# Optimization experiments

Hardware: AMD Instinct MI355X
Metric: run time of the kernel (lower is better)

Reference implementation:

```python
import jax, jax.numpy as jnp
import numpy as np

N = 100000      # num vertices
NE = 20000      # num hyperedges
NNZ = 1600000   # incidence pairs
NFEAT = 128
NHID = 64       # nhid * nhead = 8 * 8
NCLASS = 40
NLAYER = 4
ALPHA = 0.1
LAMDA = 0.5


def setup_inputs() -> dict:
    key = jax.random.key(0)
    ks = jax.random.split(key, 9)
    x = jax.random.normal(ks[0], (N, NFEAT), dtype=jnp.float32)
    vertex = jax.random.randint(ks[1], (NNZ,), 0, N, dtype=jnp.int32)
    edges = jax.random.randint(ks[2], (NNZ,), 0, NE, dtype=jnp.int32)
    degE = jax.random.uniform(ks[3], (NE, 1), dtype=jnp.float32)
    degV = jax.random.uniform(ks[4], (N, 1), dtype=jnp.float32)
    W0 = jax.random.normal(ks[5], (NFEAT, NHID), dtype=jnp.float32) * 0.05
    b0 = jnp.zeros((NHID,), jnp.float32)
    Ws = jax.random.normal(ks[6], (NLAYER, NHID, NHID), dtype=jnp.float32) * 0.05
    Wout = jax.random.normal(ks[7], (NHID, NCLASS), dtype=jnp.float32) * 0.05
    bout = jnp.zeros((NCLASS,), jnp.float32)
    return dict(x=x, degE=degE, degV=degV, W0=W0, b0=b0, Ws=Ws,
                Wout=Wout, bout=bout, vertex=vertex, edges=edges)


def _normalize_l2(X):
    # torch: norm computed on detached X, inf scales zeroed
    norm = jnp.linalg.norm(jax.lax.stop_gradient(X), axis=1, keepdims=True)
    scale = jnp.where(norm > 0, 1.0 / norm, 0.0)
    return X * scale


def reference(x, degE, degV, W0, b0, Ws, Wout, bout, vertex, edges):
    # per-hyperedge member counts for the 'mean' first_aggregate
    counts = jax.ops.segment_sum(jnp.ones((NNZ,), x.dtype), edges, num_segments=NE)
    counts = jnp.maximum(counts, 1.0)[:, None]  # [NE,1]

    X = jax.nn.relu(x @ W0 + b0)   # [N, NHID]
    X0 = X
    for i in range(NLAYER):
        beta = float(np.log(LAMDA / (i + 1) + 1.0))
        Xve = X[vertex]                                                   # [NNZ, NHID]
        Xe = jax.ops.segment_sum(Xve, edges, num_segments=NE) / counts   # vertex->edge mean
        Xe = Xe * degE                                                    # [NE, NHID]
        Xev = Xe[edges]                                                   # [NNZ, NHID]
        Xv = jax.ops.segment_sum(Xev, vertex, num_segments=N) * degV     # edge->vertex sum
        Xn = _normalize_l2(Xv)                                            # use_norm=True
        Xi = (1.0 - ALPHA) * Xn + ALPHA * X0
        X = jax.nn.relu((1.0 - beta) * Xi + beta * (Xi @ Ws[i]))
    logits = X @ Wout + bout
    return jax.nn.log_softmax(logits, axis=1)
```

## Files before the change

kernel.cpp:

```cpp
#include <hip/hip_runtime.h>
#include <math.h>

constexpr int NV   = 100000;
constexpr int NEg  = 20000;
constexpr int NNZp = 1600000;
constexpr int NF   = 128;
constexpr int NH   = 64;
constexpr int NC   = 40;

constexpr int WE  = 64;
constexpr int NBE = (NEg + WE - 1) / WE;
constexpr int WV  = 256;
constexpr int NBV = (NV + WV - 1) / WV;
constexpr int CAPS = 6400;
constexpr int CH   = 2048;
constexpr int PBLK = (NNZp + CH - 1) / CH;

typedef __bf16 bf16x8 __attribute__((ext_vector_type(8)));
typedef float  f32x4  __attribute__((ext_vector_type(4)));

__device__ __forceinline__ float bf2f(unsigned short u) {
    unsigned int x = ((unsigned int)u) << 16;
    return __builtin_bit_cast(float, x);
}
__device__ __forceinline__ unsigned short f2bf(float f) {
    unsigned int x = __builtin_bit_cast(unsigned int, f);
    x += 0x7fffu + ((x >> 16) & 1u);
    return (unsigned short)(x >> 16);
}
__device__ __forceinline__ ushort4 pack4(float a, float b, float c, float d) {
    ushort4 u; u.x = f2bf(a); u.y = f2bf(b); u.z = f2bf(c); u.w = f2bf(d);
    return u;
}

__global__ __launch_bounds__(256) void coarse_hist(const int* __restrict__ vertex,
                                                   const int* __restrict__ edges,
                                                   int* __restrict__ cnt_be,
                                                   int* __restrict__ cnt_bv) {
    __shared__ int he[NBE], hv[NBV];
    for (int i = threadIdx.x; i < NBE; i += 256) he[i] = 0;
    for (int i = threadIdx.x; i < NBV; i += 256) hv[i] = 0;
    __syncthreads();
    const int base = blockIdx.x * CH;
    const int end  = min(base + CH, NNZp);
    for (int i = base + threadIdx.x; i < end; i += 256) {
        atomicAdd(&he[edges[i]  >> 6], 1);
        atomicAdd(&hv[vertex[i] >> 8], 1);
    }
    __syncthreads();
    for (int i = threadIdx.x; i < NBE; i += 256) if (he[i]) atomicAdd(&cnt_be[i], he[i]);
    for (int i = threadIdx.x; i < NBV; i += 256) if (hv[i]) atomicAdd(&cnt_bv[i], hv[i]);
}

__global__ __launch_bounds__(512) void scan_buckets(const int* __restrict__ cnt_be,
                                                    const int* __restrict__ cnt_bv,
                                                    int* __restrict__ rsb_e,
                                                    int* __restrict__ rsb_v,
                                                    int* __restrict__ rs_e,
                                                    int* __restrict__ rs_v) {
    __shared__ int s[512];
    const int n      = (blockIdx.x == 0) ? NBE : NBV;
    const int* c     = (blockIdx.x == 0) ? cnt_be : cnt_bv;
    int* r           = (blockIdx.x == 0) ? rsb_e : rsb_v;
    const int t = threadIdx.x;
    int v = (t < n) ? c[t] : 0;
    s[t] = v;
    __syncthreads();
    for (int o = 1; o < 512; o <<= 1) {
        int u = (t >= o) ? s[t - o] : 0;
        __syncthreads();
        s[t] += u;
        __syncthreads();
    }
    if (t < n) r[t] = s[t] - v;
    if (t == 0) {
        r[n] = NNZp;
        if (blockIdx.x == 0) rs_e[NEg] = NNZp;
        else                 rs_v[NV]  = NNZp;
    }
}

__global__ __launch_bounds__(256) void partition_both(const int* __restrict__ vertex,
                                                      const int* __restrict__ edges,
                                                      const int* __restrict__ rsb_e,
                                                      const int* __restrict__ rsb_v,
                                                      int* __restrict__ gcur_e,
                                                      int* __restrict__ gcur_v,
                                                      int* __restrict__ vid_out,
                                                      int* __restrict__ eid_out) {
    __shared__ int se[CH], sv[CH];
    __shared__ int cur_e[NBE], cur_v[NBV];
    const int tid = threadIdx.x;
    for (int i = tid; i < NBE; i += 256) cur_e[i] = 0;
    for (int i = tid; i < NBV; i += 256) cur_v[i] = 0;
    __syncthreads();
    const int base = blockIdx.x * CH;
    const int n    = min(base + CH, NNZp) - base;
    for (int i = tid; i < n; i += 256) {
        int e = edges[base + i];
        int v = vertex[base + i];
        se[i] = e; sv[i] = v;
        atomicAdd(&cur_e[e >> 6], 1);
        atomicAdd(&cur_v[v >> 8], 1);
    }
    __syncthreads();
    for (int i = tid; i < NBE; i += 256) {
        int h = cur_e[i];
        cur_e[i] = rsb_e[i] + (h ? atomicAdd(&gcur_e[i], h) : 0);
    }
    for (int i = tid; i < NBV; i += 256) {
        int h = cur_v[i];
        cur_v[i] = rsb_v[i] + (h ? atomicAdd(&gcur_v[i], h) : 0);
    }
    __syncthreads();
    for (int i = tid; i < n; i += 256) {
        int e = se[i], v = sv[i];
        int pe = atomicAdd(&cur_e[e >> 6], 1);
        vid_out[pe] = (v << 6) | (e & 63);
        int pv = atomicAdd(&cur_v[v >> 8], 1);
        eid_out[pv] = (e << 8) | (v & 255);
    }
}

__global__ __launch_bounds__(512) void local_sort_both(const int* __restrict__ rsb_e,
                                                       const int* __restrict__ rsb_v,
                                                       int* __restrict__ vid_buf,
                                                       int* __restrict__ eid_buf,
                                                       int* __restrict__ rs_e,
                                                       int* __restrict__ rs_v,
                                                       const float* __restrict__ degE,
                                                       float* __restrict__ scaleE) {
    __shared__ int stage[CAPS];
    __shared__ int hist[256], off[256], cnt2[256];
    const bool eside = blockIdx.x < NBE;
    const int b   = eside ? blockIdx.x : blockIdx.x - NBE;
    const int W   = eside ? 64 : 256;
    const int FB  = eside ? 6 : 8;
    const int NID = eside ? NEg : NV;
    const int* rsb = eside ? rsb_e : rsb_v;
    int* buf       = eside ? vid_buf : eid_buf;
    int* rs        = eside ? rs_e : rs_v;
    const int base = rsb[b];
    const int sz   = rsb[b + 1] - base;
    const int tid = threadIdx.x;
    if (tid < 256) { hist[tid] = 0; cnt2[tid] = 0; }
    __syncthreads();
    for (int t = tid; t < sz; t += 512) atomicAdd(&hist[buf[base + t] & (W - 1)], 1);
    __syncthreads();
    {
        int v = (tid < W) ? hist[tid] : 0;
        if (tid < W) off[tid] = v;
        __syncthreads();
        for (int o = 1; o < W; o <<= 1) {
            int u = (tid < W && tid >= o) ? off[tid - o] : 0;
            __syncthreads();
            if (tid < W) off[tid] += u;
            __syncthreads();
        }
        if (tid < W) off[tid] -= v;
    }
    if (tid < W) {
        int gid = b * W + tid;
        if (gid < NID) {
            rs[gid] = base + off[tid];
            if (eside) {
                int c = hist[tid];
                scaleE[gid] = degE[gid] / (float)(c < 1 ? 1 : c);
            }
        }
    }
    __syncthreads();
    for (int t = tid; t < sz; t += 512) {
        int w = buf[base + t];
        int f = w & (W - 1);
        int rk = off[f] + atomicAdd(&cnt2[f], 1);
        stage[rk] = w >> FB;
    }
    __syncthreads();
    for (int t = tid; t < sz; t += 512) buf[base + t] = stage[t];
}

__global__ __launch_bounds__(256) void make_wfrag(const float* __restrict__ Ws,
                                                  const float* __restrict__ Wout,
                                                  const float* __restrict__ W0,
                                                  unsigned short* __restrict__ frag) {
    int t = blockIdx.x * 256 + threadIdx.x;
    int lane = t & 63;
    int g = t >> 6;
    int quad = lane >> 4, cl = lane & 15;
    unsigned short o[8];
    if (g < 32) {
        int li = g >> 3, w = (g >> 1) & 3, kh = g & 1;
        int n = w * 16 + cl;
#pragma unroll
        for (int j = 0; j < 8; ++j) {
            int k = kh * 32 + quad * 8 + j;
            o[j] = f2bf(Ws[(size_t)li * NH * NH + k * NH + n]);
        }
    } else if (g < 40) {
        int w = (g - 32) >> 1, kh = g & 1;
        int n = w * 16 + cl;
#pragma unroll
        for (int j = 0; j < 8; ++j) {
            int k = kh * 32 + quad * 8 + j;
            o[j] = (n < NC) ? f2bf(Wout[k * NC + n]) : (unsigned short)0;
        }
    } else {
        int w = (g - 40) >> 2, kb = (g - 40) & 3;
        int n = w * 16 + cl;
#pragma unroll
        for (int j = 0; j < 8; ++j) {
            int k = kb * 32 + quad * 8 + j;
            o[j] = f2bf(W0[k * NH + n]);
        }
    }
    unsigned short* dst = frag + (size_t)g * 512 + lane * 8;
    *((ushort4*)dst)       = *(ushort4*)&o[0];
    *((ushort4*)(dst + 4)) = *(ushort4*)&o[4];
}

__global__ __launch_bounds__(256) void gemm0_kernel(const float* __restrict__ x,
                                                    const unsigned short* __restrict__ W0frag,
                                                    const float* __restrict__ b0,
                                                    unsigned short* __restrict__ Xbf,
                                                    unsigned short* __restrict__ X0bf) {
    __shared__ unsigned short xs[16][136];
    const int tid = threadIdx.x;
    const int r  = tid >> 4;
    const int c8 = (tid & 15) * 8;
    const int rowbase = blockIdx.x * 16;
    float4 p0 = *((const float4*)(x + (size_t)(rowbase + r) * NF + c8));
    float4 p1 = *((const float4*)(x + (size_t)(rowbase + r) * NF + c8 + 4));
    *((ushort4*)&xs[r][c8])     = pack4(p0.x, p0.y, p0.z, p0.w);
    *((ushort4*)&xs[r][c8 + 4]) = pack4(p1.x, p1.y, p1.z, p1.w);
    __syncthreads();
    const int lane = tid & 63;
    const int wv   = tid >> 6;
    const int quad = lane >> 4;
    const int cl   = lane & 15;
    f32x4 acc = {0.f, 0.f, 0.f, 0.f};
#pragma unroll
    for (int kb = 0; kb < 4; ++kb) {
        bf16x8 a = *((const bf16x8*)&xs[cl][kb * 32 + quad * 8]);
        bf16x8 b = *((const bf16x8*)(W0frag + ((size_t)(wv * 4 + kb) * 64 + lane) * 8));
        acc = __builtin_amdgcn_mfma_f32_16x16x32_bf16(a, b, acc, 0, 0, 0);
    }
    const int col = wv * 16 + cl;
    const float bo = b0[col];
#pragma unroll
    for (int p = 0; p < 4; ++p) {
        const int orow = quad * 4 + p;
        float o = acc[p] + bo;
        o = o > 0.f ? o : 0.f;
        unsigned short ob = f2bf(o);
        const size_t idx = (size_t)(rowbase + orow) * NH + col;
        Xbf[idx]  = ob;
        X0bf[idx] = ob;
    }
}

__global__ __launch_bounds__(256) void gather_ve(const int* __restrict__ rs_e,
                                                 const int* __restrict__ vid_sorted,
                                                 const unsigned short* __restrict__ Xbf,
                                                 const float* __restrict__ scaleE,
                                                 unsigned short* __restrict__ Xebf) {
    const int tid = threadIdx.x;
    const int l16 = tid & 15;
    const int e = blockIdx.x * 16 + (tid >> 4);
    const int b  = rs_e[e];
    const int en = rs_e[e + 1];
    const float s = scaleE[e];
    float ax = 0.f, ay = 0.f, az = 0.f, aw = 0.f;
    int m = b;
    if (m + 4 <= en) {
        int i0 = vid_sorted[m], i1 = vid_sorted[m + 1];
        int i2 = vid_sorted[m + 2], i3 = vid_sorted[m + 3];
        m += 4;
        while (m + 4 <= en) {
            int j0 = vid_sorted[m], j1 = vid_sorted[m + 1];
            int j2 = vid_sorted[m + 2], j3 = vid_sorted[m + 3];
            m += 4;
            ushort4 p = *((const ushort4*)(Xbf + (size_t)i0 * NH) + l16);
            ushort4 q = *((const ushort4*)(Xbf + (size_t)i1 * NH) + l16);
            ushort4 u = *((const ushort4*)(Xbf + (size_t)i2 * NH) + l16);
            ushort4 t = *((const ushort4*)(Xbf + (size_t)i3 * NH) + l16);
            ax += bf2f(p.x) + bf2f(q.x) + bf2f(u.x) + bf2f(t.x);
            ay += bf2f(p.y) + bf2f(q.y) + bf2f(u.y) + bf2f(t.y);
            az += bf2f(p.z) + bf2f(q.z) + bf2f(u.z) + bf2f(t.z);
            aw += bf2f(p.w) + bf2f(q.w) + bf2f(u.w) + bf2f(t.w);
            i0 = j0; i1 = j1; i2 = j2; i3 = j3;
        }
        ushort4 p = *((const ushort4*)(Xbf + (size_t)i0 * NH) + l16);
        ushort4 q = *((const ushort4*)(Xbf + (size_t)i1 * NH) + l16);
        ushort4 u = *((const ushort4*)(Xbf + (size_t)i2 * NH) + l16);
        ushort4 t = *((const ushort4*)(Xbf + (size_t)i3 * NH) + l16);
        ax += bf2f(p.x) + bf2f(q.x) + bf2f(u.x) + bf2f(t.x);
        ay += bf2f(p.y) + bf2f(q.y) + bf2f(u.y) + bf2f(t.y);
        az += bf2f(p.z) + bf2f(q.z) + bf2f(u.z) + bf2f(t.z);
        aw += bf2f(p.w) + bf2f(q.w) + bf2f(u.w) + bf2f(t.w);
    }
    for (; m < en; ++m) {
        ushort4 p = *((const ushort4*)(Xbf + (size_t)vid_sorted[m] * NH) + l16);
        ax += bf2f(p.x); ay += bf2f(p.y); az += bf2f(p.z); aw += bf2f(p.w);
    }
    *((ushort4*)(Xebf + (size_t)e * NH) + l16) = pack4(ax * s, ay * s, az * s, aw * s);
}

template <bool LAST>
__global__ __launch_bounds__(256) void gather_ev_update(const int* __restrict__ rs_v,
                                                        const int* __restrict__ eid_sorted,
                                                        const unsigned short* __restrict__ Xebf,
                                                        const float* __restrict__ degV,
                                                        const unsigned short* __restrict__ X0bf,
                                                        const unsigned short* __restrict__ WfragL,
                                                        unsigned short* __restrict__ Xbf,
                                                        float beta,
                                                        const unsigned short* __restrict__ WfragH,
                                                        const float* __restrict__ bout,
                                                        float* __restrict__ outp) {
    __shared__ unsigned short xis_bf[16][72];
    __shared__ unsigned short xo_bf[LAST ? 16 * 72 : 1];
    __shared__ float lg[LAST ? 16 * 48 : 1];
    const int tid = threadIdx.x;
    const int l16 = tid & 15;
    const int r   = tid >> 4;
    const int v = blockIdx.x * 16 + r;
    const int b  = rs_v[v];
    const int en = rs_v[v + 1];
    const float dv = degV[v];
    float ax = 0.f, ay = 0.f, az = 0.f, aw = 0.f;
    int m = b;
    if (m + 4 <= en) {
        int i0 = eid_sorted[m], i1 = eid_sorted[m + 1];
        int i2 = eid_sorted[m + 2], i3 = eid_sorted[m + 3];
        m += 4;
        while (m + 4 <= en) {
            int j0 = eid_sorted[m], j1 = eid_sorted[m + 1];
            int j2 = eid_sorted[m + 2], j3 = eid_sorted[m + 3];
            m += 4;
            ushort4 p = *((const ushort4*)(Xebf + (size_t)i0 * NH) + l16);
            ushort4 q = *((const ushort4*)(Xebf + (size_t)i1 * NH) + l16);
            ushort4 u = *((const ushort4*)(Xebf + (size_t)i2 * NH) + l16);
            ushort4 t = *((const ushort4*)(Xebf + (size_t)i3 * NH) + l16);
            ax += bf2f(p.x) + bf2f(q.x) + bf2f(u.x) + bf2f(t.x);
            ay += bf2f(p.y) + bf2f(q.y) + bf2f(u.y) + bf2f(t.y);
            az += bf2f(p.z) + bf2f(q.z) + bf2f(u.z) + bf2f(t.z);
            aw += bf2f(p.w) + bf2f(q.w) + bf2f(u.w) + bf2f(t.w);
            i0 = j0; i1 = j1; i2 = j2; i3 = j3;
        }
        ushort4 p = *((const ushort4*)(Xebf + (size_t)i0 * NH) + l16);
        ushort4 q = *((const ushort4*)(Xebf + (size_t)i1 * NH) + l16);
        ushort4 u = *((const ushort4*)(Xebf + (size_t)i2 * NH) + l16);
        ushort4 t = *((const ushort4*)(Xebf + (size_t)i3 * NH) + l16);
        ax += bf2f(p.x) + bf2f(q.x) + bf2f(u.x) + bf2f(t.x);
        ay += bf2f(p.y) + bf2f(q.y) + bf2f(u.y) + bf2f(t.y);
        az += bf2f(p.z) + bf2f(q.z) + bf2f(u.z) + bf2f(t.z);
        aw += bf2f(p.w) + bf2f(q.w) + bf2f(u.w) + bf2f(t.w);
    }
    for (; m < en; ++m) {
        ushort4 p = *((const ushort4*)(Xebf + (size_t)eid_sorted[m] * NH) + l16);
        ax += bf2f(p.x); ay += bf2f(p.y); az += bf2f(p.z); aw += bf2f(p.w);
    }
    ax *= dv; ay *= dv; az *= dv; aw *= dv;
    float sq = ax * ax + ay * ay + az * az + aw * aw;
#pragma unroll
    for (int o = 1; o < 16; o <<= 1) sq += __shfl_xor(sq, o);
    float norm = sqrtf(sq);
    float inv = norm > 0.f ? 1.f / norm : 0.f;
    ushort4 u0 = *((const ushort4*)(X0bf + (size_t)v * NH) + l16);
    float xi0 = 0.9f * ax * inv + 0.1f * bf2f(u0.x);
    float xi1 = 0.9f * ay * inv + 0.1f * bf2f(u0.y);
    float xi2 = 0.9f * az * inv + 0.1f * bf2f(u0.z);
    float xi3 = 0.9f * aw * inv + 0.1f * bf2f(u0.w);
    *((ushort4*)&xis_bf[r][l16 * 4]) = pack4(xi0, xi1, xi2, xi3);
    __syncthreads();

    const int lane = tid & 63;
    const int wv   = tid >> 6;
    const int quad = lane >> 4;
    const int cl   = lane & 15;
    bf16x8 bw0 = *((const bf16x8*)(WfragL + ((size_t)(wv * 2 + 0) * 64 + lane) * 8));
    bf16x8 bw1 = *((const bf16x8*)(WfragL + ((size_t)(wv * 2 + 1) * 64 + lane) * 8));
    bf16x8 a0 = *((const bf16x8*)&xis_bf[cl][quad * 8]);
    bf16x8 a1 = *((const bf16x8*)&xis_bf[cl][32 + quad * 8]);
    f32x4 acc = {0.f, 0.f, 0.f, 0.f};
    acc = __builtin_amdgcn_mfma_f32_16x16x32_bf16(a0, bw0, acc, 0, 0, 0);
    acc = __builtin_amdgcn_mfma_f32_16x16x32_bf16(a1, bw1, acc, 0, 0, 0);

    const float ob = 1.f - beta;
    const int col = wv * 16 + cl;
#pragma unroll
    for (int p = 0; p < 4; ++p) {
        const int row = quad * 4 + p;
        float xiv = bf2f(xis_bf[row][col]);
        float o = ob * xiv + beta * acc[p];
        o = o > 0.f ? o : 0.f;
        if (!LAST) {
            Xbf[(size_t)(blockIdx.x * 16 + row) * NH + col] = f2bf(o);
        } else {
            xo_bf[row * 72 + col] = f2bf(o);
        }
    }
    if (LAST) {
        __syncthreads();
        bf16x8 bh0 = *((const bf16x8*)(WfragH + ((size_t)(wv * 2 + 0) * 64 + lane) * 8));
        bf16x8 bh1 = *((const bf16x8*)(WfragH + ((size_t)(wv * 2 + 1) * 64 + lane) * 8));
        bf16x8 ah0 = *((const bf16x8*)&xo_bf[cl * 72 + quad * 8]);
        bf16x8 ah1 = *((const bf16x8*)&xo_bf[cl * 72 + 32 + quad * 8]);
        f32x4 acch = {0.f, 0.f, 0.f, 0.f};
        acch = __builtin_amdgcn_mfma_f32_16x16x32_bf16(ah0, bh0, acch, 0, 0, 0);
        acch = __builtin_amdgcn_mfma_f32_16x16x32_bf16(ah1, bh1, acch, 0, 0, 0);
        if (col < NC) {
            float bo = bout[col];
#pragma unroll
            for (int p = 0; p < 4; ++p) lg[(quad * 4 + p) * 48 + col] = acch[p] + bo;
        }
        __syncthreads();
        const int r0 = wv * 4;
        const bool act = lane < NC;
        float a0s = act ? lg[(r0 + 0) * 48 + lane] : -INFINITY;
        float a1s = act ? lg[(r0 + 1) * 48 + lane] : -INFINITY;
        float a2s = act ? lg[(r0 + 2) * 48 + lane] : -INFINITY;
        float a3s = act ? lg[(r0 + 3) * 48 + lane] : -INFINITY;
        float m0 = a0s, m1 = a1s, m2 = a2s, m3 = a3s;
#pragma unroll
        for (int o = 32; o; o >>= 1) {
            m0 = fmaxf(m0, __shfl_xor(m0, o));
            m1 = fmaxf(m1, __shfl_xor(m1, o));
            m2 = fmaxf(m2, __shfl_xor(m2, o));
            m3 = fmaxf(m3, __shfl_xor(m3, o));
        }
        float e0 = act ? expf(a0s - m0) : 0.f;
        float e1 = act ? expf(a1s - m1) : 0.f;
        float e2 = act ? expf(a2s - m2) : 0.f;
        float e3 = act ? expf(a3s - m3) : 0.f;
#pragma unroll
        for (int o = 32; o; o >>= 1) {
            e0 += __shfl_xor(e0, o);
            e1 += __shfl_xor(e1, o);
            e2 += __shfl_xor(e2, o);
            e3 += __shfl_xor(e3, o);
        }
        if (act) {
            const size_t vb = (size_t)(blockIdx.x * 16 + r0) * NC + lane;
            outp[vb + 0 * NC] = a0s - m0 - logf(e0);
            outp[vb + 1 * NC] = a1s - m1 - logf(e1);
            outp[vb + 2 * NC] = a2s - m2 - logf(e2);
            outp[vb + 3 * NC] = a3s - m3 - logf(e3);
        }
    }
}

extern "C" void kernel_launch(void* const* d_in, const int* in_sizes, int n_in,
                              void* d_out, int out_size, void* d_ws, size_t ws_size,
                              hipStream_t stream) {
    const float* x    = (const float*)d_in[0];
    const float* degE = (const float*)d_in[1];
    const float* degV = (const float*)d_in[2];
    const float* W0   = (const float*)d_in[3];
    const float* b0   = (const float*)d_in[4];
    const float* Ws   = (const float*)d_in[5];
    const float* Wout = (const float*)d_in[6];
    const float* bout = (const float*)d_in[7];
    const int* vertex = (const int*)d_in[8];
    const int* edges  = (const int*)d_in[9];
    float* out = (float*)d_out;

    float* scaleE = (float*)d_ws;
    unsigned short* Xbf  = (unsigned short*)(scaleE + NEg);
    unsigned short* X0bf = Xbf + (size_t)NV * NH;
    unsigned short* Xebf = X0bf + (size_t)NV * NH;
    int* cnt_be = (int*)(Xebf + (size_t)NEg * NH);
    int* cnt_bv = cnt_be + NBE;
    int* gcur_e = cnt_bv + NBV;
    int* gcur_v = gcur_e + NBE;
    int* rsb_e  = gcur_v + NBV;
    int* rsb_v  = rsb_e + (NBE + 1);
    int* rs_e   = rsb_v + (NBV + 1);
    int* rs_v   = rs_e + (NEg + 1);
    int* vid_sorted = rs_v + (NV + 1);
    int* eid_sorted = vid_sorted + NNZp;
    unsigned short* Wfrag = (unsigned short*)(eid_sorted + NNZp);

    hipMemsetAsync(cnt_be, 0, (size_t)(NBE + NBV) * 2 * sizeof(int), stream);
    make_wfrag<<<14, 256, 0, stream>>>(Ws, Wout, W0, Wfrag);
    coarse_hist<<<PBLK, 256, 0, stream>>>(vertex, edges, cnt_be, cnt_bv);
    scan_buckets<<<2, 512, 0, stream>>>(cnt_be, cnt_bv, rsb_e, rsb_v, rs_e, rs_v);
    partition_both<<<PBLK, 256, 0, stream>>>(vertex, edges, rsb_e, rsb_v,
                                             gcur_e, gcur_v, vid_sorted, eid_sorted);
    local_sort_both<<<NBE + NBV, 512, 0, stream>>>(rsb_e, rsb_v, vid_sorted, eid_sorted,
                                                   rs_e, rs_v, degE, scaleE);

    gemm0_kernel<<<NV / 16, 256, 0, stream>>>(x, Wfrag + 40 * 512, b0, Xbf, X0bf);

    const float betas[4] = {logf(0.5f / 1.f + 1.f), logf(0.5f / 2.f + 1.f),
                            logf(0.5f / 3.f + 1.f), logf(0.5f / 4.f + 1.f)};

    for (int i = 0; i < 3; ++i) {
        gather_ve<<<NEg / 16, 256, 0, stream>>>(rs_e, vid_sorted, Xbf, scaleE, Xebf);
        gather_ev_update<false><<<NV / 16, 256, 0, stream>>>(rs_v, eid_sorted, Xebf, degV,
                                                             X0bf, Wfrag + (size_t)i * 4096,
                                                             Xbf, betas[i],
                                                             nullptr, nullptr, nullptr);
    }
    gather_ve<<<NEg / 16, 256, 0, stream>>>(rs_e, vid_sorted, Xbf, scaleE, Xebf);
    gather_ev_update<true><<<NV / 16, 256, 0, stream>>>(rs_v, eid_sorted, Xebf, degV,
                                                        X0bf, Wfrag + (size_t)3 * 4096,
                                                        Xbf, betas[3],
                                                        Wfrag + 16384, bout, out);
}
```

Measured before the change: 453.5 us.

## Stage partition scatter in LDS and widen gather loads to 16-byte vectors

The partition kernel now builds a local per-bucket ordering in shared memory using an exclusive scan and writes elements out grouped by destination bucket, aiming for more contiguous global scatter writes. It also moves to 512-thread blocks with a larger chunk size. The two gather kernels switch from 8-byte to 16-byte bf16 loads per lane, splitting each row's neighbour list between two half-groups that are combined with a shuffle. The trade-offs are more shared memory in the partition kernel and fewer lanes per row in flight during the gathers.

Result: faster. 391.1 us (-13.8%).

```diff
diff --git a/kernel.cpp b/kernel.cpp
--- a/kernel.cpp
+++ b/kernel.cpp
@@ -13,11 +13,12 @@
 constexpr int WV  = 256;
 constexpr int NBV = (NV + WV - 1) / WV;
 constexpr int CAPS = 6400;
-constexpr int CH   = 2048;
+constexpr int CH   = 4096;
 constexpr int PBLK = (NNZp + CH - 1) / CH;
 
 typedef __bf16 bf16x8 __attribute__((ext_vector_type(8)));
 typedef float  f32x4  __attribute__((ext_vector_type(4)));
+typedef unsigned short u16x8 __attribute__((ext_vector_type(8)));
 
 __device__ __forceinline__ float bf2f(unsigned short u) {
     unsigned int x = ((unsigned int)u) << 16;
@@ -31,6 +32,23 @@
 __device__ __forceinline__ ushort4 pack4(float a, float b, float c, float d) {
     ushort4 u; u.x = f2bf(a); u.y = f2bf(b); u.z = f2bf(c); u.w = f2bf(d);
     return u;
+}
+
+__device__ __forceinline__ int block_excl_scan(int val, int tid, int* wtot) {
+    __syncthreads();
+    int x = val;
+#pragma unroll
+    for (int o = 1; o < 64; o <<= 1) {
+        int y = __shfl_up(x, o);
+        if ((tid & 63) >= o) x += y;
+    }
+    if ((tid & 63) == 63) wtot[tid >> 6] = x;
+    __syncthreads();
+    int add = 0;
+    const int w = tid >> 6;
+#pragma unroll
+    for (int k = 0; k < 7; ++k) add += (k < w) ? wtot[k] : 0;
+    return add + x - val;
 }
 
 __global__ __launch_bounds__(256) void coarse_hist(const int* __restrict__ vertex,
@@ -80,7 +98,7 @@
     }
 }
 
-__global__ __launch_bounds__(256) void partition_both(const int* __restrict__ vertex,
+__global__ __launch_bounds__(512) void partition_both(const int* __restrict__ vertex,
                                                       const int* __restrict__ edges,
                                                       const int* __restrict__ rsb_e,
                                                       const int* __restrict__ rsb_v,
@@ -88,37 +106,57 @@
                                                       int* __restrict__ gcur_v,
                                                       int* __restrict__ vid_out,
                                                       int* __restrict__ eid_out) {
-    __shared__ int se[CH], sv[CH];
-    __shared__ int cur_e[NBE], cur_v[NBV];
+    __shared__ int sval_e[CH], sdst_e[CH];
+    __shared__ int sval_v[CH], sdst_v[CH];
+    __shared__ int hist_e[NBE], off_e[NBE], gbase_e[NBE], cnt_e[NBE];
+    __shared__ int hist_v[NBV], off_v[NBV], gbase_v[NBV], cnt_v[NBV];
+    __shared__ int wtot[8];
     const int tid = threadIdx.x;
-    for (int i = tid; i < NBE; i += 256) cur_e[i] = 0;
-    for (int i = tid; i < NBV; i += 256) cur_v[i] = 0;
+    for (int i = tid; i < NBE; i += 512) { hist_e[i] = 0; cnt_e[i] = 0; }
+    for (int i = tid; i < NBV; i += 512) { hist_v[i] = 0; cnt_v[i] = 0; }
     __syncthreads();
     const int base = blockIdx.x * CH;
     const int n    = min(base + CH, NNZp) - base;
-    for (int i = tid; i < n; i += 256) {
+    for (int i = tid; i < n; i += 512) {
+        atomicAdd(&hist_e[edges[base + i]  >> 6], 1);
+        atomicAdd(&hist_v[vertex[base + i] >> 8], 1);
+    }
+    __syncthreads();
+    {
+        int hv_ = (tid < NBE) ? hist_e[tid] : 0;
+        int ex  = block_excl_scan(hv_, tid, wtot);
+        if (tid < NBE) {
+            off_e[tid]   = ex;
+            gbase_e[tid] = rsb_e[tid] + (hv_ ? atomicAdd(&gcur_e[tid], hv_) : 0);
+        }
+    }
+    {
+        int hv_ = (tid < NBV) ? hist_v[tid] : 0;
+        int ex  = block_excl_scan(hv_, tid, wtot);
+        if (tid < NBV) {
+            off_v[tid]   = ex;
+            gbase_v[tid] = rsb_v[tid] + (hv_ ? atomicAdd(&gcur_v[tid], hv_) : 0);
+        }
+    }
+    __syncthreads();
+    for (int i = tid; i < n; i += 512) {
         int e = edges[base + i];
         int v = vertex[base + i];
-        se[i] = e; sv[i] = v;
-        atomicAdd(&cur_e[e >> 6], 1);
-        atomicAdd(&cur_v[v >> 8], 1);
-    }
-    __syncthreads();
-    for (int i = tid; i < NBE; i += 256) {
-        int h = cur_e[i];
-        cur_e[i] = rsb_e[i] + (h ? atomicAdd(&gcur_e[i], h) : 0);
-    }
-    for (int i = tid; i < NBV; i += 256) {
-        int h = cur_v[i];
-        cur_v[i] = rsb_v[i] + (h ? atomicAdd(&gcur_v[i], h) : 0);
-    }
-    __syncthreads();
-    for (int i = tid; i < n; i += 256) {
-        int e = se[i], v = sv[i];
-        int pe = atomicAdd(&cur_e[e >> 6], 1);
-        vid_out[pe] = (v << 6) | (e & 63);
-        int pv = atomicAdd(&cur_v[v >> 8], 1);
-        eid_out[pv] = (e << 8) | (v & 255);
+        int fe = e >> 6;
+        int rk = atomicAdd(&cnt_e[fe], 1);
+        int sl = off_e[fe] + rk;
+        sval_e[sl] = (v << 6) | (e & 63);
+        sdst_e[sl] = gbase_e[fe] + rk;
+        int fv = v >> 8;
+        int rv = atomicAdd(&cnt_v[fv], 1);
+        int s2 = off_v[fv] + rv;
+        sval_v[s2] = (e << 8) | (v & 255);
+        sdst_v[s2] = gbase_v[fv] + rv;
+    }
+    __syncthreads();
+    for (int i = tid; i < n; i += 512) {
+        vid_out[sdst_e[i]] = sval_e[i];
+        eid_out[sdst_v[i]] = sval_v[i];
     }
 }
 
@@ -265,13 +303,14 @@
                                                  const float* __restrict__ scaleE,
                                                  unsigned short* __restrict__ Xebf) {
     const int tid = threadIdx.x;
-    const int l16 = tid & 15;
+    const int l8  = tid & 7;
     const int e = blockIdx.x * 16 + (tid >> 4);
-    const int b  = rs_e[e];
-    const int en = rs_e[e + 1];
-    const float s = scaleE[e];
-    float ax = 0.f, ay = 0.f, az = 0.f, aw = 0.f;
-    int m = b;
+    const int sb = rs_e[e];
+    const int se = rs_e[e + 1];
+    const int h  = (se - sb + 1) >> 1;
+    int m        = sb + ((tid & 8) ? h : 0);
+    const int en = (tid & 8) ? se : (sb + h);
+    float a[8] = {0.f, 0.f, 0.f, 0.f, 0.f, 0.f, 0.f, 0.f};
     if (m + 4 <= en) {
         int i0 = vid_sorted[m], i1 = vid_sorted[m + 1];
         int i2 = vid_sorted[m + 2], i3 = vid_sorted[m + 3];
@@ -280,30 +319,37 @@
             int j0 = vid_sorted[m], j1 = vid_sorted[m + 1];
             int j2 = vid_sorted[m + 2], j3 = vid_sorted[m + 3];
             m += 4;
-            ushort4 p = *((const ushort4*)(Xbf + (size_t)i0 * NH) + l16);
-            ushort4 q = *((const ushort4*)(Xbf + (size_t)i1 * NH) + l16);
-            ushort4 u = *((const ushort4*)(Xbf + (size_t)i2 * NH) + l16);
-            ushort4 t = *((const ushort4*)(Xbf + (size_t)i3 * NH) + l16);
-            ax += bf2f(p.x) + bf2f(q.x) + bf2f(u.x) + bf2f(t.x);
-            ay += bf2f(p.y) + bf2f(q.y) + bf2f(u.y) + bf2f(t.y);
-            az += bf2f(p.z) + bf2f(q.z) + bf2f(u.z) + bf2f(t.z);
-            aw += bf2f(p.w) + bf2f(q.w) + bf2f(u.w) + bf2f(t.w);
+            u16x8 p = *((const u16x8*)(Xbf + (size_t)i0 * NH) + l8);
+            u16x8 q = *((const u16x8*)(Xbf + (size_t)i1 * NH) + l8);
+            u16x8 u = *((const u16x8*)(Xbf + (size_t)i2 * NH) + l8);
+            u16x8 t = *((const u16x8*)(Xbf + (size_t)i3 * NH) + l8);
+#pragma unroll
+            for (int j = 0; j < 8; ++j)
+                a[j] += bf2f(p[j]) + bf2f(q[j]) + bf2f(u[j]) + bf2f(t[j]);
             i0 = j0; i1 = j1; i2 = j2; i3 = j3;
         }
-        ushort4 p = *((const ushort4*)(Xbf + (size_t)i0 * NH) + l16);
-        ushort4 q = *((const ushort4*)(Xbf + (size_t)i1 * NH) + l16);
-        ushort4 u = *((const ushort4*)(Xbf + (size_t)i2 * NH) + l16);
-        ushort4 t = *((const ushort4*)(Xbf + (size_t)i3 * NH) + l16);
-        ax += bf2f(p.x) + bf2f(q.x) + bf2f(u.x) + bf2f(t.x);
-        ay += bf2f(p.y) + bf2f(q.y) + bf2f(u.y) + bf2f(t.y);
-        az += bf2f(p.z) + bf2f(q.z) + bf2f(u.z) + bf2f(t.z);
-        aw += bf2f(p.w) + bf2f(q.w) + bf2f(u.w) + bf2f(t.w);
+        u16x8 p = *((const u16x8*)(Xbf + (size_t)i0 * NH) + l8);
+        u16x8 q = *((const u16x8*)(Xbf + (size_t)i1 * NH) + l8);
+        u16x8 u = *((const u16x8*)(Xbf + (size_t)i2 * NH) + l8);
+        u16x8 t = *((const u16x8*)(Xbf + (size_t)i3 * NH) + l8);
+#pragma unroll
+        for (int j = 0; j < 8; ++j)
+            a[j] += bf2f(p[j]) + bf2f(q[j]) + bf2f(u[j]) + bf2f(t[j]);
     }
     for (; m < en; ++m) {
-        ushort4 p = *((const ushort4*)(Xbf + (size_t)vid_sorted[m] * NH) + l16);
-        ax += bf2f(p.x); ay += bf2f(p.y); az += bf2f(p.z); aw += bf2f(p.w);
-    }
-    *((ushort4*)(Xebf + (size_t)e * NH) + l16) = pack4(ax * s, ay * s, az * s, aw * s);
+        u16x8 p = *((const u16x8*)(Xbf + (size_t)vid_sorted[m] * NH) + l8);
+#pragma unroll
+        for (int j = 0; j < 8; ++j) a[j] += bf2f(p[j]);
+    }
+#pragma unroll
+    for (int j = 0; j < 8; ++j) a[j] += __shfl_xor(a[j], 8);
+    if (!(tid & 8)) {
+        const float s = scaleE[e];
+        u16x8 o;
+#pragma unroll
+        for (int j = 0; j < 8; ++j) o[j] = f2bf(a[j] * s);
+        *((u16x8*)(Xebf + (size_t)e * NH) + l8) = o;
+    }
 }
 
 template <bool LAST>
@@ -322,14 +368,16 @@
     __shared__ unsigned short xo_bf[LAST ? 16 * 72 : 1];
     __shared__ float lg[LAST ? 16 * 48 : 1];
     const int tid = threadIdx.x;
-    const int l16 = tid & 15;
+    const int l8  = tid & 7;
     const int r   = tid >> 4;
     const int v = blockIdx.x * 16 + r;
-    const int b  = rs_v[v];
-    const int en = rs_v[v + 1];
+    const int sb  = rs_v[v];
+    const int sen = rs_v[v + 1];
     const float dv = degV[v];
-    float ax = 0.f, ay = 0.f, az = 0.f, aw = 0.f;
-    int m = b;
+    const int h  = (sen - sb + 1) >> 1;
+    int m        = sb + ((tid & 8) ? h : 0);
+    const int en = (tid & 8) ? sen : (sb + h);
+    float a[8] = {0.f, 0.f, 0.f, 0.f, 0.f, 0.f, 0.f, 0.f};
     if (m + 4 <= en) {
         int i0 = eid_sorted[m], i1 = eid_sorted[m + 1];
         int i2 = eid_sorted[m + 2], i3 = eid_sorted[m + 3];
@@ -338,41 +386,48 @@
             int j0 = eid_sorted[m], j1 = eid_sorted[m + 1];
             int j2 = eid_sorted[m + 2], j3 = eid_sorted[m + 3];
             m += 4;
-            ushort4 p = *((const ushort4*)(Xebf + (size_t)i0 * NH) + l16);
-            ushort4 q = *((const ushort4*)(Xebf + (size_t)i1 * NH) + l16);
-            ushort4 u = *((const ushort4*)(Xebf + (size_t)i2 * NH) + l16);
-            ushort4 t = *((const ushort4*)(Xebf + (size_t)i3 * NH) + l16);
-            ax += bf2f(p.x) + bf2f(q.x) + bf2f(u.x) + bf2f(t.x);
-            ay += bf2f(p.y) + bf2f(q.y) + bf2f(u.y) + bf2f(t.y);
-            az += bf2f(p.z) + bf2f(q.z) + bf2f(u.z) + bf2f(t.z);
-            aw += bf2f(p.w) + bf2f(q.w) + bf2f(u.w) + bf2f(t.w);
+            u16x8 p = *((const u16x8*)(Xebf + (size_t)i0 * NH) + l8);
+            u16x8 q = *((const u16x8*)(Xebf + (size_t)i1 * NH) + l8);
+            u16x8 u = *((const u16x8*)(Xebf + (size_t)i2 * NH) + l8);
+            u16x8 t = *((const u16x8*)(Xebf + (size_t)i3 * NH) + l8);
+#pragma unroll
+            for (int j = 0; j < 8; ++j)
+                a[j] += bf2f(p[j]) + bf2f(q[j]) + bf2f(u[j]) + bf2f(t[j]);
             i0 = j0; i1 = j1; i2 = j2; i3 = j3;
         }
-        ushort4 p = *((const ushort4*)(Xebf + (size_t)i0 * NH) + l16);
-        ushort4 q = *((const ushort4*)(Xebf + (size_t)i1 * NH) + l16);
-        ushort4 u = *((const ushort4*)(Xebf + (size_t)i2 * NH) + l16);
-        ushort4 t = *((const ushort4*)(Xebf + (size_t)i3 * NH) + l16);
-        ax += bf2f(p.x) + bf2f(q.x) + bf2f(u.x) + bf2f(t.x);
-        ay += bf2f(p.y) + bf2f(q.y) + bf2f(u.y) + bf2f(t.y);
-        az += bf2f(p.z) + bf2f(q.z) + bf2f(u.z) + bf2f(t.z);
-        aw += bf2f(p.w) + bf2f(q.w) + bf2f(u.w) + bf2f(t.w);
+        u16x8 p = *((const u16x8*)(Xebf + (size_t)i0 * NH) + l8);
+        u16x8 q = *((const u16x8*)(Xebf + (size_t)i1 * NH) + l8);
+        u16x8 u = *((const u16x8*)(Xebf + (size_t)i2 * NH) + l8);
+        u16x8 t = *((const u16x8*)(Xebf + (size_t)i3 * NH) + l8);
+#pragma unroll
+        for (int j = 0; j < 8; ++j)
+            a[j] += bf2f(p[j]) + bf2f(q[j]) + bf2f(u[j]) + bf2f(t[j]);
     }
     for (; m < en; ++m) {
-        ushort4 p = *((const ushort4*)(Xebf + (size_t)eid_sorted[m] * NH) + l16);
-        ax += bf2f(p.x); ay += bf2f(p.y); az += bf2f(p.z); aw += bf2f(p.w);
-    }
-    ax *= dv; ay *= dv; az *= dv; aw *= dv;
-    float sq = ax * ax + ay * ay + az * az + aw * aw;
-#pragma unroll
-    for (int o = 1; o < 16; o <<= 1) sq += __shfl_xor(sq, o);
+        u16x8 p = *((const u16x8*)(Xebf + (size_t)eid_sorted[m] * NH) + l8);
+#pragma unroll
+        for (int j = 0; j < 8; ++j) a[j] += bf2f(p[j]);
+    }
+#pragma unroll
+    for (int j = 0; j < 8; ++j) {
+        a[j] += __shfl_xor(a[j], 8);
+        a[j] *= dv;
+    }
+    float sq = 0.f;
+#pragma unroll
+    for (int j = 0; j < 8; ++j) sq += a[j] * a[j];
+    sq += __shfl_xor(sq, 1);
+    sq += __shfl_xor(sq, 2);
+    sq += __shfl_xor(sq, 4);
     float norm = sqrtf(sq);
     float inv = norm > 0.f ? 1.f / norm : 0.f;
-    ushort4 u0 = *((const ushort4*)(X0bf + (size_t)v * NH) + l16);
-    float xi0 = 0.9f * ax * inv + 0.1f * bf2f(u0.x);
-    float xi1 = 0.9f * ay * inv + 0.1f * bf2f(u0.y);
-    float xi2 = 0.9f * az * inv + 0.1f * bf2f(u0.z);
-    float xi3 = 0.9f * aw * inv + 0.1f * bf2f(u0.w);
-    *((ushort4*)&xis_bf[r][l16 * 4]) = pack4(xi0, xi1, xi2, xi3);
+    u16x8 u0 = *((const u16x8*)(X0bf + (size_t)v * NH) + l8);
+    if (!(tid & 8)) {
+        u16x8 o;
+#pragma unroll
+        for (int j = 0; j < 8; ++j) o[j] = f2bf(0.9f * a[j] * inv + 0.1f * bf2f(u0[j]));
+        *((u16x8*)&xis_bf[r][l8 * 8]) = o;
+    }
     __syncthreads();
 
     const int lane = tid & 63;
@@ -486,7 +541,7 @@
     make_wfrag<<<14, 256, 0, stream>>>(Ws, Wout, W0, Wfrag);
     coarse_hist<<<PBLK, 256, 0, stream>>>(vertex, edges, cnt_be, cnt_bv);
     scan_buckets<<<2, 512, 0, stream>>>(cnt_be, cnt_bv, rsb_e, rsb_v, rs_e, rs_v);
-    partition_both<<<PBLK, 256, 0, stream>>>(vertex, edges, rsb_e, rsb_v,
+    partition_both<<<PBLK, 512, 0, stream>>>(vertex, edges, rsb_e, rsb_v,
                                              gcur_e, gcur_v, vid_sorted, eid_sorted);
     local_sort_both<<<NBE + NBV, 512, 0, stream>>>(rsb_e, rsb_v, vid_sorted, eid_sorted,
                                                    rs_e, rs_v, degE, scaleE);
```
